# Kernel optimization log

Measured on AMD Instinct MI355X. Metric: run time of the kernel, lower is better.

The kernel has to match this reference:

```python
import jax, jax.numpy as jnp
import numpy as np

TOP_K = 2


def setup_inputs() -> dict:
    key = jax.random.key(0)
    k1, k2, k3, k4 = jax.random.split(key, 4)
    B, S, D, F, E = 4, 512, 512, 2048, 16
    hidden_states = jax.random.normal(k1, (B, S, D), dtype=jnp.float32)
    gate_weight = jax.random.normal(k2, (E, D), dtype=jnp.float32) * 0.02
    w1 = jax.random.normal(k3, (E, F, D), dtype=jnp.float32) * 0.02
    w2 = jax.random.normal(k4, (E, D, F), dtype=jnp.float32) * 0.02
    return {"hidden_states": hidden_states, "gate_weight": gate_weight, "w1": w1, "w2": w2}


def reference(hidden_states, gate_weight, w1, w2):
    B, S, D = hidden_states.shape
    E = gate_weight.shape[0]
    x = hidden_states.reshape(-1, D)  # [T, D]

    # fused_top_k_routing: logits = x @ Wg^T, top-k, softmax over the k values
    gate_logits = x @ gate_weight.T  # [T, E]
    top_vals, top_idx = jax.lax.top_k(gate_logits, TOP_K)  # [T, k]
    routing_w = jax.nn.softmax(top_vals, axis=-1)  # [T, k]

    # _prepare_expert_inputs: token t goes to expert e iff e in its top-k
    mask = jnp.any(top_idx[:, :, None] == jnp.arange(E)[None, None, :], axis=1)  # [T, E] bool

    # Expert FFN on routed tokens, computed densely over (token, expert) pairs then masked.
    # h[t,e,f] = silu(x_t @ W1_e^T)
    h = jax.nn.silu(jnp.einsum('td,efd->tef', x, w1))  # [T, E, F]
    counts = jnp.sum(mask, axis=0)  # [E]
    h_sum = jnp.einsum('tef,te->ef', h, mask.astype(h.dtype))  # [E, F]
    h_mean = h_sum / jnp.maximum(counts, 1)[:, None].astype(h.dtype)

    # fused_expert_scatter_gather uses expert_outputs[e].mean(dim=0);
    # mean(W2 @ act) = W2 @ mean(act) since W2 is linear.
    y_mean = jnp.einsum('ef,edf->ed', h_mean, w2)  # [E, D]
    y_mean = jnp.where((counts > 0)[:, None], y_mean, 0.0)

    # per-token combine: sum_k w_k * mean_output[expert_k]
    out = jnp.einsum('tk,tkd->td', routing_w, y_mean[top_idx])  # [T, D]
    return out.reshape(B, S, D)
```

## Files before the change

### kernel.cpp

```cpp
#include <hip/hip_runtime.h>

#define NTOK   2048
#define DIM    512
#define FDIM   2048
#define NEXP   16
#define CAP    384
#define BT2    128
#define NTB    (CAP / BT2)

typedef __bf16 bf16x8 __attribute__((ext_vector_type(8)));
typedef float  floatx4 __attribute__((ext_vector_type(4)));

#define WS_COUNTS    0
#define WS_TOPIDX    4096
#define WS_ROUTW     20480
#define WS_HMEAN     36864
#define WS_YMEAN     167936
#define WS_XG        200704
#define WS_ZERO_BYTES 167936


__global__ __launch_bounds__(256) void k1_route_gather(
    const float* __restrict__ x, const float* __restrict__ gw,
    int* __restrict__ counts, int* __restrict__ top_idx,
    float* __restrict__ routw, __bf16* __restrict__ Xg)
{
    __shared__ float xt[16 * DIM];
    __shared__ float lg[16][17];
    __shared__ int   gde[16][2];
    __shared__ int   gdp[16][2];
    const int tid = threadIdx.x;
    const int t0  = blockIdx.x * 16;

    {
        const float4* src = (const float4*)(x + (size_t)t0 * DIM);
        float4* dst = (float4*)xt;
        #pragma unroll
        for (int i = 0; i < 8; ++i) dst[i * 256 + tid] = src[i * 256 + tid];
    }
    __syncthreads();

    {
        const int tl = tid >> 4, e = tid & 15;
        const float4* xr = (const float4*)(xt + tl * DIM);
        const float4* gr = (const float4*)(gw + e * DIM);
        float acc0 = 0.f, acc1 = 0.f;
        #pragma unroll 8
        for (int j = 0; j < DIM / 4; j += 2) {
            float4 a = xr[j],     b = gr[j];
            float4 c = xr[j + 1], d = gr[j + 1];
            acc0 += a.x * b.x + a.y * b.y + a.z * b.z + a.w * b.w;
            acc1 += c.x * d.x + c.y * d.y + c.z * d.z + c.w * d.w;
        }
        lg[tl][e] = acc0 + acc1;
    }
    __syncthreads();

    if (tid < 16) {
        const int tl = tid;
        float v0 = -1e30f, v1 = -1e30f; int i0 = 0, i1 = 0;
        #pragma unroll
        for (int e = 0; e < NEXP; ++e) {
            float v = lg[tl][e];
            if (v > v0)      { v1 = v0; i1 = i0; v0 = v; i0 = e; }
            else if (v > v1) { v1 = v;  i1 = e; }
        }
        float e1 = __expf(v1 - v0);
        float w0 = 1.f / (1.f + e1);
        float w1 = 1.f - w0;
        const int t = t0 + tl;
        top_idx[t * 2]     = i0; top_idx[t * 2 + 1] = i1;
        routw[t * 2]       = w0; routw[t * 2 + 1]   = w1;
        int p0 = atomicAdd(counts + i0, 1);
        int p1 = atomicAdd(counts + i1, 1);
        gde[tl][0] = (p0 < CAP) ? i0 : -1;  gdp[tl][0] = p0;
        gde[tl][1] = (p1 < CAP) ? i1 : -1;  gdp[tl][1] = p1;
    }
    __syncthreads();

    #pragma unroll
    for (int it = 0; it < 8; ++it) {
        int j   = it * 256 + tid;
        int row = j >> 6, s = j & 63;
        int tl  = row >> 1, k = row & 1;
        int e   = gde[tl][k];
        if (e >= 0) {
            int p = gdp[tl][k];
            const float* srcf = xt + tl * DIM + s * 8;
            float4 a = *(const float4*)srcf;
            float4 b = *(const float4*)(srcf + 4);
            bf16x8 v;
            v[0] = (__bf16)a.x; v[1] = (__bf16)a.y; v[2] = (__bf16)a.z; v[3] = (__bf16)a.w;
            v[4] = (__bf16)b.x; v[5] = (__bf16)b.y; v[6] = (__bf16)b.z; v[7] = (__bf16)b.w;
            *(bf16x8*)(Xg + ((size_t)(e * 64 + s) * CAP + p) * 8) = v;
        }
    }
}

__global__ __launch_bounds__(256, 2) void k2_expert_ffn(
    const float* __restrict__ w1, const __bf16* __restrict__ Xg,
    const int* __restrict__ counts, float* __restrict__ hmean)
{
    __shared__ __align__(16) __bf16 As[16 * 257 * 8];
    __shared__ float hred[64][2];

    const int tid = threadIdx.x;
    const int bid = blockIdx.x;
    const int tb  = bid >> 9;
    const int rem9 = bid & 511;
    const int e   = rem9 & 15;
    const int f0  = (rem9 >> 4) * 64;
    const int cnt = min(counts[e], CAP);
    if (tb * BT2 >= cnt) return;
    const float inv = 1.f / (float)cnt;

    const int wv   = tid >> 6;
    const int lane = tid & 63;
    const int q    = lane >> 4;
    const int l15  = lane & 15;
    const int fsub = (wv & 1) * 32;
    const int tsub = (wv >> 1) * 64;

    #pragma unroll
    for (int it = 0; it < 16; ++it) {
        int sg = it * 256 + tid;
        int fl = sg >> 6, sl = sg & 63;
        const float* src = w1 + ((size_t)(e * FDIM + f0 + fl)) * DIM + sl * 8;
        float4 a = ((const float4*)src)[0];
        float4 b = ((const float4*)src)[1];
        bf16x8 v;
        v[0] = (__bf16)a.x; v[1] = (__bf16)a.y; v[2] = (__bf16)a.z; v[3] = (__bf16)a.w;
        v[4] = (__bf16)b.x; v[5] = (__bf16)b.y; v[6] = (__bf16)b.z; v[7] = (__bf16)b.w;
        int kg = sl >> 2, qq = sl & 3;
        *(bf16x8*)(As + ((size_t)(kg * 257 + fl * 4 + qq)) * 8) = v;
    }
    __syncthreads();

    const __bf16* a0l = As + ((size_t)((fsub + l15) * 4 + q)) * 8;
    const __bf16* a1l = a0l + (size_t)16 * 4 * 8;
    const __bf16* bp0 = Xg + ((size_t)(e * 64 + q) * CAP + tb * BT2 + tsub + l15) * 8;

    floatx4 acc[2][4];
    #pragma unroll
    for (int a = 0; a < 2; ++a)
        #pragma unroll
        for (int b = 0; b < 4; ++b) acc[a][b] = (floatx4)0.f;

    #pragma unroll
    for (int kg = 0; kg < 16; ++kg) {
        bf16x8 af0 = *(const bf16x8*)(a0l + (size_t)kg * 257 * 8);
        bf16x8 af1 = *(const bf16x8*)(a1l + (size_t)kg * 257 * 8);
        const __bf16* bp = bp0 + (size_t)kg * 4 * CAP * 8;
        #pragma unroll
        for (int tt = 0; tt < 4; ++tt) {
            bf16x8 bv = *(const bf16x8*)(bp + tt * 16 * 8);
            acc[0][tt] = __builtin_amdgcn_mfma_f32_16x16x32_bf16(af0, bv, acc[0][tt], 0, 0, 0);
            acc[1][tt] = __builtin_amdgcn_mfma_f32_16x16x32_bf16(af1, bv, acc[1][tt], 0, 0, 0);
        }
    }

    float hs[8];
    #pragma unroll
    for (int i = 0; i < 8; ++i) hs[i] = 0.f;
    #pragma unroll
    for (int fa = 0; fa < 2; ++fa)
        #pragma unroll
        for (int tt = 0; tt < 4; ++tt)
            #pragma unroll
            for (int r = 0; r < 4; ++r) {
                float v = acc[fa][tt][r];
                hs[fa * 4 + r] += v / (1.f + __expf(-v));
            }

    #pragma unroll
    for (int i = 0; i < 8; ++i) {
        float v = hs[i];
        v += __shfl_xor(v, 1);
        v += __shfl_xor(v, 2);
        v += __shfl_xor(v, 4);
        v += __shfl_xor(v, 8);
        hs[i] = v;
    }
    if (l15 == 0) {
        #pragma unroll
        for (int fa = 0; fa < 2; ++fa)
            #pragma unroll
            for (int r = 0; r < 4; ++r) {
                int row = fsub + fa * 16 + q * 4 + r;
                hred[row][wv >> 1] = hs[fa * 4 + r];
            }
    }
    __syncthreads();
    if (tid < 64)
        atomicAdd(hmean + (size_t)e * FDIM + f0 + tid,
                  (hred[tid][0] + hred[tid][1]) * inv);
}

__global__ __launch_bounds__(256) void k3_ymean(
    const float* __restrict__ w2, const float* __restrict__ hmean,
    const int* __restrict__ counts, float* __restrict__ ymean)
{
    __shared__ float hl[FDIM];
    const int tid = threadIdx.x;
    const int bid = blockIdx.x;
    const int e   = bid >> 7;
    const int d0  = (bid & 127) * 4;

    {
        const float4* hg = (const float4*)(hmean + (size_t)e * FDIM);
        float4* hl4 = (float4*)hl;
        hl4[tid]       = hg[tid];
        hl4[256 + tid] = hg[256 + tid];
    }
    __syncthreads();

    const int wv = tid >> 6, lane = tid & 63;
    const int d = d0 + wv;
    const float4* wr  = (const float4*)(w2 + ((size_t)e * DIM + d) * FDIM);
    const float4* hl4 = (const float4*)hl;
    float acc = 0.f;
    #pragma unroll
    for (int i = 0; i < 8; ++i) {
        float4 a = wr[i * 64 + lane];
        float4 h = hl4[i * 64 + lane];
        acc += a.x * h.x + a.y * h.y + a.z * h.z + a.w * h.w;
    }
    #pragma unroll
    for (int m = 1; m < 64; m <<= 1) acc += __shfl_xor(acc, m);
    if (lane == 0)
        ymean[e * DIM + d] = (counts[e] > 0) ? acc : 0.f;
}

__global__ __launch_bounds__(256) void k4_combine(
    const int* __restrict__ top_idx, const float* __restrict__ routw,
    const float* __restrict__ ymean, float* __restrict__ out)
{
    const int idx = blockIdx.x * 256 + threadIdx.x;
    const int t = idx >> 7;
    const int c = idx & 127;
    const int i0 = top_idx[t * 2], i1 = top_idx[t * 2 + 1];
    const float w0 = routw[t * 2], w1 = routw[t * 2 + 1];
    float4 a = ((const float4*)(ymean + (size_t)i0 * DIM))[c];
    float4 b = ((const float4*)(ymean + (size_t)i1 * DIM))[c];
    float4 o;
    o.x = w0 * a.x + w1 * b.x;
    o.y = w0 * a.y + w1 * b.y;
    o.z = w0 * a.z + w1 * b.z;
    o.w = w0 * a.w + w1 * b.w;
    ((float4*)out)[idx] = o;
}

extern "C" void kernel_launch(void* const* d_in, const int* in_sizes, int n_in,
                              void* d_out, int out_size, void* d_ws, size_t ws_size,
                              hipStream_t stream)
{
    (void)in_sizes; (void)n_in; (void)out_size; (void)ws_size;
    const float* x  = (const float*)d_in[0];
    const float* gw = (const float*)d_in[1];
    const float* w1 = (const float*)d_in[2];
    const float* w2 = (const float*)d_in[3];
    float* out = (float*)d_out;

    char* ws = (char*)d_ws;
    int*    counts  = (int*)   (ws + WS_COUNTS);
    int*    top_idx = (int*)   (ws + WS_TOPIDX);
    float*  routw   = (float*) (ws + WS_ROUTW);
    float*  hmean   = (float*) (ws + WS_HMEAN);
    float*  ymean   = (float*) (ws + WS_YMEAN);
    __bf16* Xg      = (__bf16*)(ws + WS_XG);

    hipMemsetAsync(d_ws, 0, WS_ZERO_BYTES, stream);

    k1_route_gather<<<dim3(NTOK / 16), dim3(256), 0, stream>>>(x, gw, counts, top_idx, routw, Xg);
    k2_expert_ffn  <<<dim3(NTB * 32 * NEXP), dim3(256), 0, stream>>>(w1, Xg, counts, hmean);
    k3_ymean       <<<dim3(NEXP * 128), dim3(256), 0, stream>>>(w2, hmean, counts, ymean);
    k4_combine     <<<dim3(NTOK * DIM / 4 / 256), dim3(256), 0, stream>>>(top_idx, routw, ymean, out);
}
```

Measured before the change: 234.7 us.

## Pre-convert w1 to swizzled bf16 and async-load tiles into LDS once per block

Adds a pre-pass kernel that converts w1 from fp32 to bf16 in an MFMA-friendly tiled layout in workspace. The FFN kernel now loads each weight tile straight into LDS with global_load_lds and loops over all token blocks of an expert inside one block, instead of launching one block per token block and reloading and converting w1 each time. This removes the repeated fp32 weight reads and conversions per token block. In exchange it adds a full conversion pass over w1 on every call, extra workspace, and fewer, longer-running blocks for the FFN kernel.

```diff
diff --git a/kernel.cpp b/kernel.cpp
--- a/kernel.cpp
+++ b/kernel.cpp
@@ -17,8 +17,42 @@
 #define WS_HMEAN     36864
 #define WS_YMEAN     167936
 #define WS_XG        200704
+#define WS_XG_BYTES  (NEXP * 64 * CAP * 16)
+#define WS_W1B       (WS_XG + WS_XG_BYTES)
+#define WS_W1B_BYTES (NEXP * FDIM * DIM * 2)
 #define WS_ZERO_BYTES 167936
 
+
+__device__ __forceinline__ void async_lds16(const void* g, void* l) {
+    __builtin_amdgcn_global_load_lds(
+        (const __attribute__((address_space(1))) void*)g,
+        (__attribute__((address_space(3))) void*)l, 16, 0, 0);
+}
+
+__global__ __launch_bounds__(256) void k0_convert(
+    const float* __restrict__ w1, __bf16* __restrict__ w1b)
+{
+    const int nthr = gridDim.x * blockDim.x;
+    int j = blockIdx.x * 256 + threadIdx.x;
+    #pragma unroll
+    for (int it = 0; it < 4; ++it, j += nthr) {
+        int flo = j & 15;
+        int q   = (j >> 4) & 3;
+        int fhi = (j >> 6) & 3;
+        int kg  = (j >> 8) & 15;
+        int ft  = (j >> 12) & 31;
+        int e   = j >> 17;
+        int f = ft * 64 + fhi * 16 + flo;
+        int d = kg * 32 + q * 8;
+        const float* src = w1 + ((size_t)(e * FDIM + f)) * DIM + d;
+        float4 a = ((const float4*)src)[0];
+        float4 b = ((const float4*)src)[1];
+        bf16x8 v;
+        v[0] = (__bf16)a.x; v[1] = (__bf16)a.y; v[2] = (__bf16)a.z; v[3] = (__bf16)a.w;
+        v[4] = (__bf16)b.x; v[5] = (__bf16)b.y; v[6] = (__bf16)b.z; v[7] = (__bf16)b.w;
+        *(bf16x8*)(w1b + (size_t)j * 8) = v;
+    }
+}
 
 __global__ __launch_bounds__(256) void k1_route_gather(
     const float* __restrict__ x, const float* __restrict__ gw,
@@ -98,21 +132,19 @@
 }
 
 __global__ __launch_bounds__(256, 2) void k2_expert_ffn(
-    const float* __restrict__ w1, const __bf16* __restrict__ Xg,
+    const __bf16* __restrict__ w1b, const __bf16* __restrict__ Xg,
     const int* __restrict__ counts, float* __restrict__ hmean)
 {
-    __shared__ __align__(16) __bf16 As[16 * 257 * 8];
+    __shared__ __align__(16) __bf16 As[16 * 256 * 8];
     __shared__ float hred[64][2];
 
     const int tid = threadIdx.x;
     const int bid = blockIdx.x;
-    const int tb  = bid >> 9;
-    const int rem9 = bid & 511;
-    const int e   = rem9 & 15;
-    const int f0  = (rem9 >> 4) * 64;
+    const int e   = bid & 15;
+    const int ft  = bid >> 4;
+    const int f0  = ft * 64;
     const int cnt = min(counts[e], CAP);
-    if (tb * BT2 >= cnt) return;
-    const float inv = 1.f / (float)cnt;
+    const float inv = 1.f / (float)max(cnt, 1);
 
     const int wv   = tid >> 6;
     const int lane = tid & 63;
@@ -120,57 +152,54 @@
     const int l15  = lane & 15;
     const int fsub = (wv & 1) * 32;
     const int tsub = (wv >> 1) * 64;
-
-    #pragma unroll
-    for (int it = 0; it < 16; ++it) {
-        int sg = it * 256 + tid;
-        int fl = sg >> 6, sl = sg & 63;
-        const float* src = w1 + ((size_t)(e * FDIM + f0 + fl)) * DIM + sl * 8;
-        float4 a = ((const float4*)src)[0];
-        float4 b = ((const float4*)src)[1];
-        bf16x8 v;
-        v[0] = (__bf16)a.x; v[1] = (__bf16)a.y; v[2] = (__bf16)a.z; v[3] = (__bf16)a.w;
-        v[4] = (__bf16)b.x; v[5] = (__bf16)b.y; v[6] = (__bf16)b.z; v[7] = (__bf16)b.w;
-        int kg = sl >> 2, qq = sl & 3;
-        *(bf16x8*)(As + ((size_t)(kg * 257 + fl * 4 + qq)) * 8) = v;
-    }
-    __syncthreads();
-
-    const __bf16* a0l = As + ((size_t)((fsub + l15) * 4 + q)) * 8;
-    const __bf16* a1l = a0l + (size_t)16 * 4 * 8;
-    const __bf16* bp0 = Xg + ((size_t)(e * 64 + q) * CAP + tb * BT2 + tsub + l15) * 8;
-
-    floatx4 acc[2][4];
-    #pragma unroll
-    for (int a = 0; a < 2; ++a)
-        #pragma unroll
-        for (int b = 0; b < 4; ++b) acc[a][b] = (floatx4)0.f;
-
-    #pragma unroll
-    for (int kg = 0; kg < 16; ++kg) {
-        bf16x8 af0 = *(const bf16x8*)(a0l + (size_t)kg * 257 * 8);
-        bf16x8 af1 = *(const bf16x8*)(a1l + (size_t)kg * 257 * 8);
-        const __bf16* bp = bp0 + (size_t)kg * 4 * CAP * 8;
-        #pragma unroll
-        for (int tt = 0; tt < 4; ++tt) {
-            bf16x8 bv = *(const bf16x8*)(bp + tt * 16 * 8);
-            acc[0][tt] = __builtin_amdgcn_mfma_f32_16x16x32_bf16(af0, bv, acc[0][tt], 0, 0, 0);
-            acc[1][tt] = __builtin_amdgcn_mfma_f32_16x16x32_bf16(af1, bv, acc[1][tt], 0, 0, 0);
+    const int wvbase = tid & 192;
+
+    const __bf16* tile = w1b + (size_t)(e * 32 + ft) * 4096 * 8;
+    #pragma unroll
+    for (int i = 0; i < 16; ++i) {
+        int s = i * 256 + wvbase;
+        async_lds16(tile + ((size_t)s + (tid & 63)) * 8, As + (size_t)s * 8);
+    }
+    __syncthreads();
+
+    const __bf16* a0l = As + ((size_t)((fsub >> 4) * 64 + lane)) * 8;
+    const __bf16* a1l = a0l + (size_t)64 * 8;
+
+    float hs[8];
+    #pragma unroll
+    for (int i = 0; i < 8; ++i) hs[i] = 0.f;
+
+    for (int tb = 0; tb < NTB; ++tb) {
+        if (tb * BT2 >= cnt) break;
+        floatx4 acc[2][4];
+        #pragma unroll
+        for (int a = 0; a < 2; ++a)
+            #pragma unroll
+            for (int b = 0; b < 4; ++b) acc[a][b] = (floatx4)0.f;
+
+        const __bf16* bp0 = Xg + ((size_t)(e * 64 + q) * CAP + tb * BT2 + tsub + l15) * 8;
+        #pragma unroll
+        for (int kg = 0; kg < 16; ++kg) {
+            bf16x8 af0 = *(const bf16x8*)(a0l + (size_t)kg * 256 * 8);
+            bf16x8 af1 = *(const bf16x8*)(a1l + (size_t)kg * 256 * 8);
+            const __bf16* bp = bp0 + (size_t)kg * 4 * CAP * 8;
+            #pragma unroll
+            for (int tt = 0; tt < 4; ++tt) {
+                bf16x8 bv = *(const bf16x8*)(bp + tt * 16 * 8);
+                acc[0][tt] = __builtin_amdgcn_mfma_f32_16x16x32_bf16(af0, bv, acc[0][tt], 0, 0, 0);
+                acc[1][tt] = __builtin_amdgcn_mfma_f32_16x16x32_bf16(af1, bv, acc[1][tt], 0, 0, 0);
+            }
         }
-    }
-
-    float hs[8];
-    #pragma unroll
-    for (int i = 0; i < 8; ++i) hs[i] = 0.f;
-    #pragma unroll
-    for (int fa = 0; fa < 2; ++fa)
-        #pragma unroll
-        for (int tt = 0; tt < 4; ++tt)
+        #pragma unroll
+        for (int fa = 0; fa < 2; ++fa)
             #pragma unroll
-            for (int r = 0; r < 4; ++r) {
-                float v = acc[fa][tt][r];
-                hs[fa * 4 + r] += v / (1.f + __expf(-v));
-            }
+            for (int tt = 0; tt < 4; ++tt)
+                #pragma unroll
+                for (int r = 0; r < 4; ++r) {
+                    float v = acc[fa][tt][r];
+                    hs[fa * 4 + r] += v / (1.f + __expf(-v));
+                }
+    }
 
     #pragma unroll
     for (int i = 0; i < 8; ++i) {
@@ -268,11 +297,13 @@
     float*  hmean   = (float*) (ws + WS_HMEAN);
     float*  ymean   = (float*) (ws + WS_YMEAN);
     __bf16* Xg      = (__bf16*)(ws + WS_XG);
+    __bf16* w1b     = (__bf16*)(ws + WS_W1B);
 
     hipMemsetAsync(d_ws, 0, WS_ZERO_BYTES, stream);
 
+    k0_convert     <<<dim3(2048), dim3(256), 0, stream>>>(w1, w1b);
     k1_route_gather<<<dim3(NTOK / 16), dim3(256), 0, stream>>>(x, gw, counts, top_idx, routw, Xg);
-    k2_expert_ffn  <<<dim3(NTB * 32 * NEXP), dim3(256), 0, stream>>>(w1, Xg, counts, hmean);
+    k2_expert_ffn  <<<dim3(32 * NEXP), dim3(256), 0, stream>>>(w1b, Xg, counts, hmean);
     k3_ymean       <<<dim3(NEXP * 128), dim3(256), 0, stream>>>(w2, hmean, counts, ymean);
     k4_combine     <<<dim3(NTOK * DIM / 4 / 256), dim3(256), 0, stream>>>(top_idx, routw, ymean, out);
 }
```

New measurement: 226.4 us. 1.04x faster.

## Keep W1 tile in registers and loop over token blocks inside expert FFN

Applied to the files above, without the earlier changes.

The expert FFN kernel now gives each block a 32-row F tile. Each wave loads its W1 fragment straight from global memory into registers once, instead of staging through shared memory, and loops over all token blocks inside the kernel. This removes the shared-memory staging and the repeated W1 reloads across token-block launches. Because each block now owns its output slice, the atomicAdd into hmean becomes a plain store, which shrinks the workspace memset. In exchange there are fewer blocks per expert and the token blocks are processed serially, and register pressure goes up (launch bounds now ask for 3 blocks per CU).

```diff
diff --git a/kernel.cpp b/kernel.cpp
--- a/kernel.cpp
+++ b/kernel.cpp
@@ -17,7 +17,7 @@
 #define WS_HMEAN     36864
 #define WS_YMEAN     167936
 #define WS_XG        200704
-#define WS_ZERO_BYTES 167936
+#define WS_ZERO_BYTES 4096
 
 
 __global__ __launch_bounds__(256) void k1_route_gather(
@@ -97,83 +97,72 @@
     }
 }
 
-__global__ __launch_bounds__(256, 2) void k2_expert_ffn(
+__global__ __launch_bounds__(256, 3) void k2_expert_ffn(
     const float* __restrict__ w1, const __bf16* __restrict__ Xg,
     const int* __restrict__ counts, float* __restrict__ hmean)
 {
-    __shared__ __align__(16) __bf16 As[16 * 257 * 8];
-    __shared__ float hred[64][2];
+    __shared__ float hred[32][2];
 
     const int tid = threadIdx.x;
     const int bid = blockIdx.x;
-    const int tb  = bid >> 9;
-    const int rem9 = bid & 511;
-    const int e   = rem9 & 15;
-    const int f0  = (rem9 >> 4) * 64;
+    const int e   = bid & 15;
+    const int ft  = bid >> 4;
+    const int f0  = ft * 32;
     const int cnt = min(counts[e], CAP);
-    if (tb * BT2 >= cnt) return;
-    const float inv = 1.f / (float)cnt;
+    const float inv = 1.f / (float)max(cnt, 1);
 
     const int wv   = tid >> 6;
     const int lane = tid & 63;
     const int q    = lane >> 4;
     const int l15  = lane & 15;
-    const int fsub = (wv & 1) * 32;
+    const int fsub = (wv & 1) * 16;
     const int tsub = (wv >> 1) * 64;
 
-    #pragma unroll
-    for (int it = 0; it < 16; ++it) {
-        int sg = it * 256 + tid;
-        int fl = sg >> 6, sl = sg & 63;
-        const float* src = w1 + ((size_t)(e * FDIM + f0 + fl)) * DIM + sl * 8;
-        float4 a = ((const float4*)src)[0];
-        float4 b = ((const float4*)src)[1];
-        bf16x8 v;
-        v[0] = (__bf16)a.x; v[1] = (__bf16)a.y; v[2] = (__bf16)a.z; v[3] = (__bf16)a.w;
-        v[4] = (__bf16)b.x; v[5] = (__bf16)b.y; v[6] = (__bf16)b.z; v[7] = (__bf16)b.w;
-        int kg = sl >> 2, qq = sl & 3;
-        *(bf16x8*)(As + ((size_t)(kg * 257 + fl * 4 + qq)) * 8) = v;
-    }
-    __syncthreads();
-
-    const __bf16* a0l = As + ((size_t)((fsub + l15) * 4 + q)) * 8;
-    const __bf16* a1l = a0l + (size_t)16 * 4 * 8;
-    const __bf16* bp0 = Xg + ((size_t)(e * 64 + q) * CAP + tb * BT2 + tsub + l15) * 8;
-
-    floatx4 acc[2][4];
-    #pragma unroll
-    for (int a = 0; a < 2; ++a)
-        #pragma unroll
-        for (int b = 0; b < 4; ++b) acc[a][b] = (floatx4)0.f;
-
-    #pragma unroll
-    for (int kg = 0; kg < 16; ++kg) {
-        bf16x8 af0 = *(const bf16x8*)(a0l + (size_t)kg * 257 * 8);
-        bf16x8 af1 = *(const bf16x8*)(a1l + (size_t)kg * 257 * 8);
-        const __bf16* bp = bp0 + (size_t)kg * 4 * CAP * 8;
-        #pragma unroll
-        for (int tt = 0; tt < 4; ++tt) {
-            bf16x8 bv = *(const bf16x8*)(bp + tt * 16 * 8);
-            acc[0][tt] = __builtin_amdgcn_mfma_f32_16x16x32_bf16(af0, bv, acc[0][tt], 0, 0, 0);
-            acc[1][tt] = __builtin_amdgcn_mfma_f32_16x16x32_bf16(af1, bv, acc[1][tt], 0, 0, 0);
-        }
-    }
-
-    float hs[8];
-    #pragma unroll
-    for (int i = 0; i < 8; ++i) hs[i] = 0.f;
-    #pragma unroll
-    for (int fa = 0; fa < 2; ++fa)
+    bf16x8 areg[16];
+    {
+        const float* ap = w1 + ((size_t)(e * FDIM + f0 + fsub + l15)) * DIM + q * 8;
+        #pragma unroll
+        for (int kg = 0; kg < 16; ++kg) {
+            float4 a = *(const float4*)(ap + kg * 32);
+            float4 b = *(const float4*)(ap + kg * 32 + 4);
+            bf16x8 v;
+            v[0] = (__bf16)a.x; v[1] = (__bf16)a.y; v[2] = (__bf16)a.z; v[3] = (__bf16)a.w;
+            v[4] = (__bf16)b.x; v[5] = (__bf16)b.y; v[6] = (__bf16)b.z; v[7] = (__bf16)b.w;
+            areg[kg] = v;
+        }
+    }
+
+    float hs[4];
+    #pragma unroll
+    for (int i = 0; i < 4; ++i) hs[i] = 0.f;
+
+    for (int tb = 0; tb < NTB; ++tb) {
+        if (tb * BT2 >= cnt) break;
+        floatx4 acc[4];
+        #pragma unroll
+        for (int b = 0; b < 4; ++b) acc[b] = (floatx4)0.f;
+
+        const __bf16* bp0 = Xg + ((size_t)(e * 64 + q) * CAP + tb * BT2 + tsub + l15) * 8;
+        #pragma unroll
+        for (int kg = 0; kg < 16; ++kg) {
+            const __bf16* bp = bp0 + (size_t)kg * 4 * CAP * 8;
+            #pragma unroll
+            for (int tt = 0; tt < 4; ++tt) {
+                bf16x8 bv = *(const bf16x8*)(bp + tt * 16 * 8);
+                acc[tt] = __builtin_amdgcn_mfma_f32_16x16x32_bf16(areg[kg], bv, acc[tt], 0, 0, 0);
+            }
+        }
         #pragma unroll
         for (int tt = 0; tt < 4; ++tt)
             #pragma unroll
             for (int r = 0; r < 4; ++r) {
-                float v = acc[fa][tt][r];
-                hs[fa * 4 + r] += v / (1.f + __expf(-v));
+                float v = acc[tt][r];
+                hs[r] += v / (1.f + __expf(-v));
             }
-
-    #pragma unroll
-    for (int i = 0; i < 8; ++i) {
+    }
+
+    #pragma unroll
+    for (int i = 0; i < 4; ++i) {
         float v = hs[i];
         v += __shfl_xor(v, 1);
         v += __shfl_xor(v, 2);
@@ -183,17 +172,12 @@
     }
     if (l15 == 0) {
         #pragma unroll
-        for (int fa = 0; fa < 2; ++fa)
-            #pragma unroll
-            for (int r = 0; r < 4; ++r) {
-                int row = fsub + fa * 16 + q * 4 + r;
-                hred[row][wv >> 1] = hs[fa * 4 + r];
-            }
-    }
-    __syncthreads();
-    if (tid < 64)
-        atomicAdd(hmean + (size_t)e * FDIM + f0 + tid,
-                  (hred[tid][0] + hred[tid][1]) * inv);
+        for (int r = 0; r < 4; ++r)
+            hred[fsub + q * 4 + r][wv >> 1] = hs[r];
+    }
+    __syncthreads();
+    if (tid < 32)
+        hmean[(size_t)e * FDIM + f0 + tid] = (hred[tid][0] + hred[tid][1]) * inv;
 }
 
 __global__ __launch_bounds__(256) void k3_ymean(
@@ -272,7 +256,7 @@
     hipMemsetAsync(d_ws, 0, WS_ZERO_BYTES, stream);
 
     k1_route_gather<<<dim3(NTOK / 16), dim3(256), 0, stream>>>(x, gw, counts, top_idx, routw, Xg);
-    k2_expert_ffn  <<<dim3(NTB * 32 * NEXP), dim3(256), 0, stream>>>(w1, Xg, counts, hmean);
+    k2_expert_ffn  <<<dim3(64 * NEXP), dim3(256), 0, stream>>>(w1, Xg, counts, hmean);
     k3_ymean       <<<dim3(NEXP * 128), dim3(256), 0, stream>>>(w2, hmean, counts, ymean);
     k4_combine     <<<dim3(NTOK * DIM / 4 / 256), dim3(256), 0, stream>>>(top_idx, routw, ymean, out);
 }
```

Measured after the change: 226.5 us. -3.5%, faster.
